# Optimization experiments

Measured on AMD Instinct MI355X. Metric: run time of the kernel, lower is better.

Reference implementation:

```python
import jax, jax.numpy as jnp
import numpy as np

T = 16384  # total training steps (length of LR schedule)
M = 8192   # number of evaluated checkpoints
HUBER_DELTA = 0.001


def _huber(delta, r):
    a = jnp.abs(r)
    return jnp.where(a <= delta, 0.5 * r * r, delta * (a - 0.5 * delta))


def setup_inputs() -> dict:
    key = jax.random.key(0)
    k1, k2, k3 = jax.random.split(key, 3)
    # realistic positive LR schedule (~3e-4), required since lrs**(-gamma) is taken
    lrs = jax.random.uniform(k1, (T,), dtype=jnp.float32) * 3e-4 + 1e-5
    lr_sum = jnp.cumsum(lrs)
    step = jnp.sort(jax.random.randint(k2, (M,), 0, T))
    S1 = lr_sum[step]  # cumulative LR sum at the evaluated steps
    # lr_gap = consecutive LR differences (delta of the schedule); index 0 unused
    lr_gap = jnp.concatenate([jnp.zeros((1,), jnp.float32), lrs[:-1] - lrs[1:]])
    loss = jax.random.uniform(k3, (M,), dtype=jnp.float32) + 2.0  # positive (log taken)
    p = lambda v: jnp.float32(v)
    return {
        "S1": S1, "lrs": lrs, "lr_sum": lr_sum, "step": step,
        "lr_gap": lr_gap, "loss": loss,
        "L0": p(2.5), "A": p(0.5), "alpha": p(0.5), "B": p(300.0),
        "C": p(1.0), "beta": p(0.5), "gamma": p(0.6),
    }


def reference(S1, lrs, lr_sum, step, lr_gap, loss, L0, A, alpha, B, C, beta, gamma):
    # Vectorized triangular reduction replacing the per-step Python loop:
    # for step s: LD = sum_{k=1..s} lr_gap[k] * (1 - (1 + C*lrs[k]^-gamma*(lr_sum[s]-lr_sum[k-1]))^-beta)
    Tn = lrs.shape[0]
    k = jnp.arange(Tn)
    mask = (k[None, :] >= 1) & (k[None, :] <= step[:, None])  # [M, T]
    lr_sum_prev = jnp.concatenate([jnp.zeros((1,), lr_sum.dtype), lr_sum[:-1]])
    G = lr_sum[step][:, None] - lr_sum_prev[None, :]          # lr_sum[s] - lr_sum[k-1]
    G = jnp.where(mask, G, 0.0)                               # keep base positive where masked
    inner = 1.0 + C * (lrs ** (-gamma))[None, :] * G          # [M, T]
    term = lr_gap[None, :] * (1.0 - inner ** (-beta))
    LD = jnp.sum(jnp.where(mask, term, 0.0), axis=1)          # [M]
    pred = L0 + A * S1 ** (-alpha) + B * LD
    r = jnp.log(loss) - jnp.log(jnp.clip(pred, 1e-10))
    return _huber(HUBER_DELTA, r).sum()
```

## Files before the change

kernel.cpp:

```cpp
#include <hip/hip_runtime.h>
#include <math.h>

#define BLK 512
#define GSZ 8
#define PAD 4
#define KSTRIDE (BLK*4)

#if __has_builtin(__builtin_amdgcn_rsqf)
#define RSQF(x) __builtin_amdgcn_rsqf(x)
#else
#define RSQF(x) (1.0f / sqrtf(x))
#endif

__device__ __forceinline__ float fast_pow(float x, float e) {
  return __expf(e * __logf(x));
}

__global__ __launch_bounds__(256) void precompute_kernel(
    const float* __restrict__ lrs, const float* __restrict__ lr_sum,
    const float* __restrict__ lr_gap,
    float* __restrict__ cpw, float* __restrict__ dd, float* __restrict__ gapp,
    const float* __restrict__ gamma_p, const float* __restrict__ C_p, int T) {
  int i = blockIdx.x * 256 + threadIdx.x;
  if (i >= T + PAD) return;
  if (i == 0 || i >= T) {
    cpw[i] = 0.0f; dd[i] = 1.0f; gapp[i] = 0.0f;
    return;
  }
  float c = C_p[0] * fast_pow(lrs[i], -gamma_p[0]);
  cpw[i]  = c;
  dd[i]   = fmaf(-c, lr_sum[i - 1], 1.0f);
  gapp[i] = lr_gap[i];
}

template <bool USE_RSQ>
__device__ __forceinline__ void ld_body(
    const float* __restrict__ cpw, const float* __restrict__ dd,
    const float* __restrict__ gapp,
    const float (&Ss)[GSZ], const int (&sv)[GSZ], float (&acc)[GSZ],
    int kEnd1, int smax, float nb) {
  int tid = threadIdx.x;

  for (int k0 = tid * 4; k0 < kEnd1; k0 += KSTRIDE) {
    float4 c4 = *(const float4*)(cpw + k0);
    float4 d4 = *(const float4*)(dd + k0);
    float4 g4 = *(const float4*)(gapp + k0);
    const float ce[4] = {c4.x, c4.y, c4.z, c4.w};
    const float de[4] = {d4.x, d4.y, d4.z, d4.w};
    const float ge[4] = {g4.x, g4.y, g4.z, g4.w};
#pragma unroll
    for (int e = 0; e < 4; ++e) {
#pragma unroll
      for (int j = 0; j < GSZ; ++j) {
        float inner = fmaf(ce[e], Ss[j], de[e]);
        float p = USE_RSQ ? RSQF(inner) : __expf(nb * __logf(inner));
        acc[j] = fmaf(ge[e], p, acc[j]);
      }
    }
  }

  for (int k0 = kEnd1 + tid * 4; k0 <= smax; k0 += KSTRIDE) {
    float4 c4 = *(const float4*)(cpw + k0);
    float4 d4 = *(const float4*)(dd + k0);
    float4 g4 = *(const float4*)(gapp + k0);
    const float ce[4] = {c4.x, c4.y, c4.z, c4.w};
    const float de[4] = {d4.x, d4.y, d4.z, d4.w};
    const float ge[4] = {g4.x, g4.y, g4.z, g4.w};
#pragma unroll
    for (int e = 0; e < 4; ++e) {
#pragma unroll
      for (int j = 0; j < GSZ; ++j) {
        float inner = fmaf(ce[e], Ss[j], de[e]);
        float p = USE_RSQ ? RSQF(inner) : __expf(nb * __logf(inner));
        float pm = (k0 + e <= sv[j]) ? p : 0.0f;
        acc[j] = fmaf(ge[e], pm, acc[j]);
      }
    }
  }
}

__global__ __launch_bounds__(BLK, 8) void ld_kernel(
    const float* __restrict__ S1, const int* __restrict__ step,
    const float* __restrict__ loss, const float* __restrict__ lrs,
    const float* __restrict__ cpw, const float* __restrict__ dd,
    const float* __restrict__ gapp,
    const float* __restrict__ L0_p, const float* __restrict__ A_p,
    const float* __restrict__ alpha_p, const float* __restrict__ B_p,
    const float* __restrict__ beta_p,
    float* __restrict__ hub, int nchunk) {
  __shared__ float wacc[BLK / 64][GSZ];

  int mbase = blockIdx.x * GSZ;

  float Ss[GSZ]; int sv[GSZ]; float acc[GSZ];
#pragma unroll
  for (int j = 0; j < GSZ; ++j) {
    Ss[j] = S1[mbase + j];
    sv[j] = step[mbase + j];
    acc[j] = 0.0f;
  }
  int smin = sv[0], smax = sv[0];
#pragma unroll
  for (int j = 1; j < GSZ; ++j) {
    smin = min(smin, sv[j]);
    smax = max(smax, sv[j]);
  }
  int kEnd1 = ((smin + 1) / KSTRIDE) * KSTRIDE;

  float beta = beta_p[0];
  float nb = -beta;

  if (beta == 0.5f)
    ld_body<true>(cpw, dd, gapp, Ss, sv, acc, kEnd1, smax, nb);
  else
    ld_body<false>(cpw, dd, gapp, Ss, sv, acc, kEnd1, smax, nb);

  int lane = threadIdx.x & 63, wid = threadIdx.x >> 6;
#pragma unroll
  for (int j = 0; j < GSZ; ++j) {
    float v = acc[j];
#pragma unroll
    for (int off = 32; off; off >>= 1) v += __shfl_down(v, off, 64);
    if (lane == 0) wacc[wid][j] = v;
  }
  __syncthreads();

  if (threadIdx.x < GSZ) {
    int j = threadIdx.x;
    int m = mbase + j;
    float sgp = 0.0f;
#pragma unroll
    for (int w = 0; w < BLK / 64; ++w) sgp += wacc[w][j];
    int s = step[m];
    float Ssum = S1[m];
    float LD = (lrs[0] - lrs[s]) - sgp;
    float pred = L0_p[0] + A_p[0] * fast_pow(Ssum, -alpha_p[0]) + B_p[0] * LD;
    pred = fmaxf(pred, 1e-10f);
    float r = __logf(loss[m]) - __logf(pred);
    float a = fabsf(r);
    const float dlt = 0.001f;
    hub[m] = (a <= dlt) ? (0.5f * r * r) : (dlt * (a - 0.5f * dlt));
  }
}

__global__ __launch_bounds__(1024) void reduce_kernel(
    const float* __restrict__ hub, float* __restrict__ out, int M) {
  float acc = 0.0f;
  for (int i = threadIdx.x; i < M; i += 1024) acc += hub[i];
#pragma unroll
  for (int off = 32; off; off >>= 1) acc += __shfl_down(acc, off, 64);
  __shared__ float wacc[16];
  int lane = threadIdx.x & 63, wid = threadIdx.x >> 6;
  if (lane == 0) wacc[wid] = acc;
  __syncthreads();
  if (threadIdx.x == 0) {
    float t = 0.0f;
#pragma unroll
    for (int i = 0; i < 16; ++i) t += wacc[i];
    out[0] = t;
  }
}

extern "C" void kernel_launch(void* const* d_in, const int* in_sizes, int n_in,
                              void* d_out, int out_size, void* d_ws, size_t ws_size,
                              hipStream_t stream) {
  const float* S1      = (const float*)d_in[0];
  const float* lrs     = (const float*)d_in[1];
  const float* lr_sum  = (const float*)d_in[2];
  const int*   step    = (const int*)  d_in[3];
  const float* lr_gap  = (const float*)d_in[4];
  const float* loss    = (const float*)d_in[5];
  const float* L0_p    = (const float*)d_in[6];
  const float* A_p     = (const float*)d_in[7];
  const float* alpha_p = (const float*)d_in[8];
  const float* B_p     = (const float*)d_in[9];
  const float* C_p     = (const float*)d_in[10];
  const float* beta_p  = (const float*)d_in[11];
  const float* gamma_p = (const float*)d_in[12];

  int M = in_sizes[0];
  int T = in_sizes[1];
  int Tp = T + PAD;

  float* cpw  = (float*)d_ws;
  float* dd   = cpw + Tp;
  float* gapp = dd + Tp;
  float* hub  = gapp + Tp;

  int nchunk = M / GSZ;

  precompute_kernel<<<(Tp + 255) / 256, 256, 0, stream>>>(
      lrs, lr_sum, lr_gap, cpw, dd, gapp, gamma_p, C_p, T);
  ld_kernel<<<nchunk, BLK, 0, stream>>>(
      S1, step, loss, lrs, cpw, dd, gapp,
      L0_p, A_p, alpha_p, B_p, beta_p, hub, nchunk);
  reduce_kernel<<<1, 1024, 0, stream>>>(hub, (float*)d_out, M);
}
```

Measured before the change: 26.90 us.

## Stage schedule arrays through double-buffered LDS tiles with direct global-to-LDS loads

Replaces per-thread direct global float4 loads of the precomputed coefficient arrays with a tiled loop that stages each 2048-element tile of all three arrays into shared memory, double-buffered, using the async global_load_lds builtin when available. Full tiles skip masking and the last partial tiles apply the per-checkpoint mask. The aim is to overlap fetching the next tile with compute on the current one. In exchange it uses 48KB of LDS per block, which limits occupancy, and adds a block barrier per tile.

```diff
diff --git a/kernel.cpp b/kernel.cpp
--- a/kernel.cpp
+++ b/kernel.cpp
@@ -3,8 +3,8 @@
 
 #define BLK 512
 #define GSZ 8
-#define PAD 4
-#define KSTRIDE (BLK*4)
+#define TILE 2048
+#define NW (BLK / 64)
 
 #if __has_builtin(__builtin_amdgcn_rsqf)
 #define RSQF(x) __builtin_amdgcn_rsqf(x)
@@ -16,13 +16,26 @@
   return __expf(e * __logf(x));
 }
 
+#if __has_builtin(__builtin_amdgcn_global_load_lds)
+__device__ __forceinline__ void gl_lds16(const float* g, float* l) {
+  __builtin_amdgcn_global_load_lds(
+      (const __attribute__((address_space(1))) uint32_t*)g,
+      (__attribute__((address_space(3))) uint32_t*)l, 16, 0, 0);
+}
+#define STAGE_ONE(src, gi, dst, lb) gl_lds16((src) + (gi), &(dst)[lb])
+#else
+#define STAGE_ONE(src, gi, dst, lb)  \
+  *(float4*)&(dst)[(gi) & (TILE - 1)] = *(const float4*)((src) + (gi))
+#endif
+
 __global__ __launch_bounds__(256) void precompute_kernel(
     const float* __restrict__ lrs, const float* __restrict__ lr_sum,
     const float* __restrict__ lr_gap,
     float* __restrict__ cpw, float* __restrict__ dd, float* __restrict__ gapp,
-    const float* __restrict__ gamma_p, const float* __restrict__ C_p, int T) {
+    const float* __restrict__ gamma_p, const float* __restrict__ C_p,
+    int T, int Tpad) {
   int i = blockIdx.x * 256 + threadIdx.x;
-  if (i >= T + PAD) return;
+  if (i >= Tpad) return;
   if (i == 0 || i >= T) {
     cpw[i] = 0.0f; dd[i] = 1.0f; gapp[i] = 0.0f;
     return;
@@ -33,49 +46,56 @@
   gapp[i] = lr_gap[i];
 }
 
+template <bool USE_RSQ, bool MASKED>
+__device__ __forceinline__ void tile_terms(
+    const float (&buf)[3][TILE], int tid, int kglob,
+    const float (&Ss)[GSZ], const int (&sv)[GSZ], float (&acc)[GSZ],
+    float nb) {
+  float4 c4 = *(const float4*)&buf[0][tid * 4];
+  float4 d4 = *(const float4*)&buf[1][tid * 4];
+  float4 g4 = *(const float4*)&buf[2][tid * 4];
+  const float ce[4] = {c4.x, c4.y, c4.z, c4.w};
+  const float de[4] = {d4.x, d4.y, d4.z, d4.w};
+  const float ge[4] = {g4.x, g4.y, g4.z, g4.w};
+#pragma unroll
+  for (int e = 0; e < 4; ++e) {
+#pragma unroll
+    for (int j = 0; j < GSZ; ++j) {
+      float inner = fmaf(ce[e], Ss[j], de[e]);
+      float p = USE_RSQ ? RSQF(inner) : __expf(nb * __logf(inner));
+      float pm = (!MASKED || (kglob + e <= sv[j])) ? p : 0.0f;
+      acc[j] = fmaf(ge[e], pm, acc[j]);
+    }
+  }
+}
+
 template <bool USE_RSQ>
-__device__ __forceinline__ void ld_body(
+__device__ __forceinline__ void ld_loop(
     const float* __restrict__ cpw, const float* __restrict__ dd,
-    const float* __restrict__ gapp,
+    const float* __restrict__ gapp, float (&lbuf)[2][3][TILE],
     const float (&Ss)[GSZ], const int (&sv)[GSZ], float (&acc)[GSZ],
-    int kEnd1, int smax, float nb) {
-  int tid = threadIdx.x;
-
-  for (int k0 = tid * 4; k0 < kEnd1; k0 += KSTRIDE) {
-    float4 c4 = *(const float4*)(cpw + k0);
-    float4 d4 = *(const float4*)(dd + k0);
-    float4 g4 = *(const float4*)(gapp + k0);
-    const float ce[4] = {c4.x, c4.y, c4.z, c4.w};
-    const float de[4] = {d4.x, d4.y, d4.z, d4.w};
-    const float ge[4] = {g4.x, g4.y, g4.z, g4.w};
-#pragma unroll
-    for (int e = 0; e < 4; ++e) {
-#pragma unroll
-      for (int j = 0; j < GSZ; ++j) {
-        float inner = fmaf(ce[e], Ss[j], de[e]);
-        float p = USE_RSQ ? RSQF(inner) : __expf(nb * __logf(inner));
-        acc[j] = fmaf(ge[e], p, acc[j]);
-      }
+    int nfull, int ntile, float nb, int tid) {
+  int lb = (tid & ~63) * 4;
+
+  STAGE_ONE(cpw,  tid * 4, lbuf[0][0], lb);
+  STAGE_ONE(dd,   tid * 4, lbuf[0][1], lb);
+  STAGE_ONE(gapp, tid * 4, lbuf[0][2], lb);
+  __syncthreads();
+
+  for (int t = 0; t < ntile; ++t) {
+    int cur = t & 1;
+    if (t + 1 < ntile) {
+      int gi = (t + 1) * TILE + tid * 4;
+      STAGE_ONE(cpw,  gi, lbuf[cur ^ 1][0], lb);
+      STAGE_ONE(dd,   gi, lbuf[cur ^ 1][1], lb);
+      STAGE_ONE(gapp, gi, lbuf[cur ^ 1][2], lb);
     }
-  }
-
-  for (int k0 = kEnd1 + tid * 4; k0 <= smax; k0 += KSTRIDE) {
-    float4 c4 = *(const float4*)(cpw + k0);
-    float4 d4 = *(const float4*)(dd + k0);
-    float4 g4 = *(const float4*)(gapp + k0);
-    const float ce[4] = {c4.x, c4.y, c4.z, c4.w};
-    const float de[4] = {d4.x, d4.y, d4.z, d4.w};
-    const float ge[4] = {g4.x, g4.y, g4.z, g4.w};
-#pragma unroll
-    for (int e = 0; e < 4; ++e) {
-#pragma unroll
-      for (int j = 0; j < GSZ; ++j) {
-        float inner = fmaf(ce[e], Ss[j], de[e]);
-        float p = USE_RSQ ? RSQF(inner) : __expf(nb * __logf(inner));
-        float pm = (k0 + e <= sv[j]) ? p : 0.0f;
-        acc[j] = fmaf(ge[e], pm, acc[j]);
-      }
-    }
+    int kglob = t * TILE + tid * 4;
+    if (t < nfull)
+      tile_terms<USE_RSQ, false>(lbuf[cur], tid, kglob, Ss, sv, acc, nb);
+    else
+      tile_terms<USE_RSQ, true>(lbuf[cur], tid, kglob, Ss, sv, acc, nb);
+    __syncthreads();
   }
 }
 
@@ -87,9 +107,11 @@
     const float* __restrict__ L0_p, const float* __restrict__ A_p,
     const float* __restrict__ alpha_p, const float* __restrict__ B_p,
     const float* __restrict__ beta_p,
-    float* __restrict__ hub, int nchunk) {
-  __shared__ float wacc[BLK / 64][GSZ];
-
+    float* __restrict__ hub) {
+  __shared__ float lbuf[2][3][TILE];
+  __shared__ float wacc[NW][GSZ];
+
+  int tid = threadIdx.x;
   int mbase = blockIdx.x * GSZ;
 
   float Ss[GSZ]; int sv[GSZ]; float acc[GSZ];
@@ -105,17 +127,18 @@
     smin = min(smin, sv[j]);
     smax = max(smax, sv[j]);
   }
-  int kEnd1 = ((smin + 1) / KSTRIDE) * KSTRIDE;
+  int nfull = (smin + 1) / TILE;
+  int ntile = smax / TILE + 1;
 
   float beta = beta_p[0];
   float nb = -beta;
 
   if (beta == 0.5f)
-    ld_body<true>(cpw, dd, gapp, Ss, sv, acc, kEnd1, smax, nb);
+    ld_loop<true>(cpw, dd, gapp, lbuf, Ss, sv, acc, nfull, ntile, nb, tid);
   else
-    ld_body<false>(cpw, dd, gapp, Ss, sv, acc, kEnd1, smax, nb);
-
-  int lane = threadIdx.x & 63, wid = threadIdx.x >> 6;
+    ld_loop<false>(cpw, dd, gapp, lbuf, Ss, sv, acc, nfull, ntile, nb, tid);
+
+  int lane = tid & 63, wid = tid >> 6;
 #pragma unroll
   for (int j = 0; j < GSZ; ++j) {
     float v = acc[j];
@@ -125,12 +148,12 @@
   }
   __syncthreads();
 
-  if (threadIdx.x < GSZ) {
-    int j = threadIdx.x;
+  if (tid < GSZ) {
+    int j = tid;
     int m = mbase + j;
     float sgp = 0.0f;
 #pragma unroll
-    for (int w = 0; w < BLK / 64; ++w) sgp += wacc[w][j];
+    for (int w = 0; w < NW; ++w) sgp += wacc[w][j];
     int s = step[m];
     float Ssum = S1[m];
     float LD = (lrs[0] - lrs[s]) - sgp;
@@ -180,19 +203,19 @@
 
   int M = in_sizes[0];
   int T = in_sizes[1];
-  int Tp = T + PAD;
+  int Tpad = ((T + TILE - 1) / TILE) * TILE;
 
   float* cpw  = (float*)d_ws;
-  float* dd   = cpw + Tp;
-  float* gapp = dd + Tp;
-  float* hub  = gapp + Tp;
+  float* dd   = cpw + Tpad;
+  float* gapp = dd + Tpad;
+  float* hub  = gapp + Tpad;
 
   int nchunk = M / GSZ;
 
-  precompute_kernel<<<(Tp + 255) / 256, 256, 0, stream>>>(
-      lrs, lr_sum, lr_gap, cpw, dd, gapp, gamma_p, C_p, T);
+  precompute_kernel<<<(Tpad + 255) / 256, 256, 0, stream>>>(
+      lrs, lr_sum, lr_gap, cpw, dd, gapp, gamma_p, C_p, T, Tpad);
   ld_kernel<<<nchunk, BLK, 0, stream>>>(
       S1, step, loss, lrs, cpw, dd, gapp,
-      L0_p, A_p, alpha_p, B_p, beta_p, hub, nchunk);
+      L0_p, A_p, alpha_p, B_p, beta_p, hub);
   reduce_kernel<<<1, 1024, 0, stream>>>(hub, (float*)d_out, M);
 }
```

Result: slower. 31.00 us (+15.2%).
